# Kernel tuning notes

Measured on AMD Instinct MI355X. Metric: run time of the kernel, lower is better.

## Reference

```python
import jax, jax.numpy as jnp
import numpy as np

NIBBLE_SHIFTS = jnp.arange(8, dtype=jnp.int32) * 4


def _unpack_int4(packed):
    # packed: [..., P] int32 -> [..., P*8] int32 values in [0, 15]
    vals = (packed[..., None] >> NIBBLE_SHIFTS) & 0xF
    return vals.reshape(*packed.shape[:-1], packed.shape[-1] * 8)


def setup_inputs() -> dict:
    key = jax.random.key(0)
    k1, k2, k3, k4, k5, k6 = jax.random.split(key, 6)
    M, K, N, G = 4096, 4096, 11008, 128
    inp = jax.random.normal(k1, (M, K), dtype=jnp.float32)
    qweight = jax.random.randint(k2, (K, N // 8), 0, 2147483647, dtype=jnp.int32)
    woq_scales = jax.random.uniform(k3, (K // G, N), dtype=jnp.float32)
    woq_qzeros = jax.random.randint(k4, (K // G, N // 8), 0, 2147483647, dtype=jnp.int32)
    woq_bias = jax.random.normal(k5, (N,), dtype=jnp.float32)
    mul = jax.random.normal(k6, (M, N), dtype=jnp.float32)
    return {"inp": inp, "qweight": qweight, "woq_scales": woq_scales,
            "woq_qzeros": woq_qzeros, "woq_bias": woq_bias, "mul": mul,
            "group_size": G}


def reference(inp, qweight, woq_scales, woq_qzeros, woq_bias, mul, group_size):
    K = qweight.shape[0]
    # dequantize int4 weights: w = (q - z) * scale, per group of `group_size` K-rows
    w_int = _unpack_int4(qweight).astype(jnp.float32)            # [K, N]
    z_int = _unpack_int4(woq_qzeros).astype(jnp.float32)         # [K/G, N]
    zeros_full = jnp.repeat(z_int, group_size, axis=0)           # [K, N]
    scales_full = jnp.repeat(woq_scales, group_size, axis=0)     # [K, N]
    w = (w_int - zeros_full) * scales_full                       # [K, N]
    woq_out = inp @ w + woq_bias                                 # [M, N]
    return jax.nn.silu(woq_out) * mul
```

## Files before the change

kernel.cpp:

```cpp
#include <hip/hip_runtime.h>
#include <hip/hip_bf16.h>

typedef __attribute__((ext_vector_type(8))) short short8;
typedef __attribute__((ext_vector_type(4))) short short4v;
typedef __attribute__((ext_vector_type(4))) float float4v;

__device__ __forceinline__ short f2bf(float f) {
  union { float f; unsigned u; } v; v.f = f;
  unsigned r = v.u + 0x7fffu + ((v.u >> 16) & 1u);
  return (short)(r >> 16);
}

typedef const __attribute__((address_space(1))) unsigned int* as1_u32p;
typedef __attribute__((address_space(3))) unsigned int* as3_u32p;

__device__ __forceinline__ void gl_lds16(const void* g, void* l) {
  __builtin_amdgcn_global_load_lds((as1_u32p)g, (as3_u32p)l, 16, 0, 0);
}

__global__ __launch_bounds__(256, 2)
void dequant_kernel(const int* __restrict__ qw,
                    const float* __restrict__ scales,
                    const int* __restrict__ qzeros,
                    short* __restrict__ Bt,
                    int K, int N, int G)
{
  __shared__ short Ls[128 * 64];
  const int N8  = N >> 3;
  const int k0  = blockIdx.x * 64;
  const int n80 = blockIdx.y * 16;
  const int g   = k0 / G;
  const int tid  = threadIdx.x;
  const int lane = tid & 63;
  const int w    = tid >> 6;

  const int4 q4 = *(const int4*)(qw + (size_t)(k0 + lane) * N8 + n80 + w * 4);
  const int4 z4 = *(const int4*)(qzeros + (size_t)g * N8 + n80 + w * 4);
  const int qa[4] = {q4.x, q4.y, q4.z, q4.w};
  const int za[4] = {z4.x, z4.y, z4.z, z4.w};

  #pragma unroll
  for (int it = 0; it < 4; ++it) {
    const int n8l = w * 4 + it;
    const float4v s0 = *(const float4v*)(scales + (size_t)g * N + (n80 + n8l) * 8);
    const float4v s1 = *(const float4v*)(scales + (size_t)g * N + (n80 + n8l) * 8 + 4);
    const float sc[8] = {s0[0], s0[1], s0[2], s0[3], s1[0], s1[1], s1[2], s1[3]};
    const int wq = qa[it], wz = za[it];
    #pragma unroll
    for (int j = 0; j < 8; ++j) {
      const float z = (float)((wz >> (4 * j)) & 0xF);
      const float q = (float)((wq >> (4 * j)) & 0xF);
      Ls[(n8l * 8 + j) * 64 + lane] = f2bf((q - z) * sc[j]);
    }
  }
  __syncthreads();

  #pragma unroll
  for (int it = 0; it < 4; ++it) {
    const int c   = tid + it * 256;
    const int row = c >> 3;
    const int off = (c & 7) * 8;
    const short8 v = *(const short8*)(&Ls[row * 64 + off]);
    *(short8*)(Bt + (size_t)(n80 * 8 + row) * K + k0 + off) = v;
  }
}

__global__ __launch_bounds__(256, 4)
void aconv_kernel(const float* __restrict__ in, short* __restrict__ out, long long n)
{
  const long long i = ((long long)blockIdx.x * blockDim.x + threadIdx.x) * 8;
  if (i >= n) return;
  const float4v a = *(const float4v*)(in + i);
  const float4v b = *(const float4v*)(in + i + 4);
  short8 h;
  h[0] = f2bf(a[0]); h[1] = f2bf(a[1]); h[2] = f2bf(a[2]); h[3] = f2bf(a[3]);
  h[4] = f2bf(b[0]); h[5] = f2bf(b[1]); h[6] = f2bf(b[2]); h[7] = f2bf(b[3]);
  *(short8*)(out + i) = h;
}

__global__ __launch_bounds__(512, 2)
void gemm256_silu_mul_kernel(const short* __restrict__ A,
                             const short* __restrict__ Bt,
                             const float* __restrict__ bias,
                             const float* __restrict__ mulp,
                             float*       __restrict__ out,
                             int M, int N, int K)
{
  __shared__ short L[2][2][16384];

  const int tid  = threadIdx.x;
  const int lane = tid & 63;
  const int wave = tid >> 6;
  const int wm   = wave >> 2;
  const int wn   = wave & 3;

  const int nwg = gridDim.x;
  const int q8 = nwg >> 3, r8 = nwg & 7;
  const int xcd = blockIdx.x & 7, sub = blockIdx.x >> 3;
  const int swz = (xcd < r8 ? xcd * (q8 + 1) : r8 * (q8 + 1) + (xcd - r8) * q8) + sub;
  const int nbx = N >> 8;
  const int bx = swz % nbx, by = swz / nbx;
  const int m0 = by << 8, n0 = bx << 8;

  const short* Ab = A  + (size_t)m0 * K;
  const short* Bb = Bt + (size_t)n0 * K;

  const int srow = lane >> 2;
  const int scol = (((lane & 3) ^ ((lane & 32) >> 4))) * 8;
  const int fm = lane & 15;
  const int ko = ((lane >> 4) * 8) ^ ((fm & 8) ? 16 : 0);

  float4v acc[8][4];
  #pragma unroll
  for (int i = 0; i < 8; ++i)
    #pragma unroll
    for (int j = 0; j < 4; ++j)
      acc[i][j] = (float4v){0.f, 0.f, 0.f, 0.f};

  const int NT = K >> 6;

  auto stage = [&](int buf, int ab, const short* __restrict__ base, int kk) {
    #pragma unroll
    for (int i = 0; i < 4; ++i) {
      const int ms = wave * 2 + (i >> 1);
      const int ks = i & 1;
      const int st = ms * 2 + ks;
      gl_lds16(base + (size_t)(ms * 16 + srow) * K + kk + ks * 32 + scol,
               &L[buf][ab][st * 512]);
    }
  };

  stage(0, 0, Ab, 0);
  stage(0, 1, Bb, 0);

  for (int t = 0; t < NT; ++t) {
    const int cur = t & 1;
    const int kk1 = (t + 1) << 6;
    const bool pf = (t + 1) < NT;

    asm volatile("s_waitcnt vmcnt(0)" ::: "memory");
    __builtin_amdgcn_s_barrier();

    #pragma unroll
    for (int qm = 0; qm < 2; ++qm) {
      short8 af[4][2];
      #pragma unroll
      for (int i = 0; i < 4; ++i)
        #pragma unroll
        for (int ks = 0; ks < 2; ++ks)
          af[i][ks] = *(const short8*)(
              &L[cur][0][((wm * 8 + qm * 4 + i) * 2 + ks) * 512 + fm * 32 + ko]);

      #pragma unroll
      for (int qn = 0; qn < 2; ++qn) {
        short8 bf[2][2];
        #pragma unroll
        for (int j = 0; j < 2; ++j)
          #pragma unroll
          for (int ks = 0; ks < 2; ++ks)
            bf[j][ks] = *(const short8*)(
                &L[cur][1][((wn * 4 + qn * 2 + j) * 2 + ks) * 512 + fm * 32 + ko]);

        if (qm == 0 && pf) {
          if (qn == 0) stage(cur ^ 1, 0, Ab, kk1);
          else         stage(cur ^ 1, 1, Bb, kk1);
        }

        __builtin_amdgcn_s_barrier();
        asm volatile("s_waitcnt lgkmcnt(0)" ::: "memory");
        __builtin_amdgcn_sched_barrier(0);
        __builtin_amdgcn_s_setprio(1);
        #pragma unroll
        for (int i = 0; i < 4; ++i)
          #pragma unroll
          for (int j = 0; j < 2; ++j)
            #pragma unroll
            for (int ks = 0; ks < 2; ++ks)
              acc[qm * 4 + i][qn * 2 + j] = __builtin_amdgcn_mfma_f32_16x16x32_bf16(
                  af[i][ks], bf[j][ks], acc[qm * 4 + i][qn * 2 + j], 0, 0, 0);
        __builtin_amdgcn_s_setprio(0);
        __builtin_amdgcn_s_barrier();
      }
    }
  }

  const int cn  = lane & 15;
  const int cr4 = (lane >> 4) * 4;
  #pragma unroll
  for (int mt = 0; mt < 8; ++mt) {
    #pragma unroll
    for (int nt = 0; nt < 4; ++nt) {
      const int n  = n0 + wn * 64 + nt * 16 + cn;
      const float bn = bias[n];
      #pragma unroll
      for (int i = 0; i < 4; ++i) {
        const int m = m0 + wm * 128 + mt * 16 + cr4 + i;
        float x = acc[mt][nt][i] + bn;
        float s = x / (1.0f + __expf(-x));
        out[(size_t)m * N + n] = s * mulp[(size_t)m * N + n];
      }
    }
  }
}

__global__ __launch_bounds__(256, 2)
void gemm_silu_mul_kernel(const short* __restrict__ A,
                          const short* __restrict__ Bt,
                          const float* __restrict__ bias,
                          const float* __restrict__ mulp,
                          float*       __restrict__ out,
                          int M, int N, int K)
{
  __shared__ short As[128 * 64];
  __shared__ short Bs[128 * 64];

  const int tid  = threadIdx.x;
  const int lane = tid & 63;
  const int wave = tid >> 6;
  const int wr = (wave >> 1) * 64;
  const int wc = (wave & 1) * 64;
  const int m0 = blockIdx.y * 128;
  const int n0 = blockIdx.x * 128;

  float4v acc[4][4];
  #pragma unroll
  for (int i = 0; i < 4; ++i)
    #pragma unroll
    for (int j = 0; j < 4; ++j)
      acc[i][j] = (float4v){0.f, 0.f, 0.f, 0.f};

  const int fm = lane & 15;
  const int fk = (lane >> 4) * 8;
  const int srow = lane >> 3;
  const int scol = (lane & 7) * 8;

  for (int k0 = 0; k0 < K; k0 += 64) {
    #pragma unroll
    for (int c = 0; c < 4; ++c) {
      const int chunk = wave * 4 + c;
      const int row   = chunk * 8 + srow;
      gl_lds16(A  + (size_t)(m0 + row) * K + k0 + scol, &As[chunk * 512]);
      gl_lds16(Bt + (size_t)(n0 + row) * K + k0 + scol, &Bs[chunk * 512]);
    }
    __syncthreads();

    #pragma unroll
    for (int ks = 0; ks < 64; ks += 32) {
      short8 a[4], b[4];
      #pragma unroll
      for (int mt = 0; mt < 4; ++mt)
        a[mt] = *(const short8*)(&As[(wr + mt * 16 + fm) * 64 + ks + fk]);
      #pragma unroll
      for (int nt = 0; nt < 4; ++nt)
        b[nt] = *(const short8*)(&Bs[(wc + nt * 16 + fm) * 64 + ks + fk]);
      #pragma unroll
      for (int mt = 0; mt < 4; ++mt)
        #pragma unroll
        for (int nt = 0; nt < 4; ++nt)
          acc[mt][nt] = __builtin_amdgcn_mfma_f32_16x16x32_bf16(a[mt], b[nt], acc[mt][nt], 0, 0, 0);
    }
    __syncthreads();
  }

  const int cn = lane & 15;
  const int cr = (lane >> 4) * 4;
  #pragma unroll
  for (int mt = 0; mt < 4; ++mt) {
    #pragma unroll
    for (int nt = 0; nt < 4; ++nt) {
      const int n  = n0 + wc + nt * 16 + cn;
      const float bn = bias[n];
      #pragma unroll
      for (int i = 0; i < 4; ++i) {
        const int m = m0 + wr + mt * 16 + cr + i;
        float x = acc[mt][nt][i] + bn;
        float s = x / (1.0f + __expf(-x));
        out[(size_t)m * N + n] = s * mulp[(size_t)m * N + n];
      }
    }
  }
}

#define BM 128
#define BN 128
#define BK 64
#define LDA 72
#define LDB 72

__global__ __launch_bounds__(256, 2)
void woq_silu_mul_kernel(const float* __restrict__ inp, const int* __restrict__ qw,
                         const float* __restrict__ scales, const int* __restrict__ qzeros,
                         const float* __restrict__ bias, const float* __restrict__ mulp,
                         float* __restrict__ out, int M, int N, int K, int G)
{
  __shared__ short As[BM * LDA];
  __shared__ short Bs[BN * LDB];
  const int tid  = threadIdx.x;
  const int lane = tid & 63;
  const int wave = tid >> 6;
  const int wr = (wave >> 1) * 64;
  const int wc = (wave & 1) * 64;
  const int m0 = blockIdx.y * BM;
  const int n0 = blockIdx.x * BN;
  const int N8 = N >> 3;
  float4v acc[4][4];
  #pragma unroll
  for (int i = 0; i < 4; ++i)
    #pragma unroll
    for (int j = 0; j < 4; ++j)
      acc[i][j] = (float4v){0.f, 0.f, 0.f, 0.f};
  const int n8l  = tid >> 4;
  const int kloc = (tid & 15) * 4;
  const int fm = lane & 15;
  const int fk = (lane >> 4) * 8;
  for (int k0 = 0; k0 < K; k0 += BK) {
    #pragma unroll
    for (int i = 0; i < 8; ++i) {
      int f = tid + i * 256;
      int row = f >> 4;
      int col = (f & 15) * 4;
      float4v a4 = *(const float4v*)(inp + (size_t)(m0 + row) * K + k0 + col);
      short4v h;
      h[0] = f2bf(a4[0]); h[1] = f2bf(a4[1]); h[2] = f2bf(a4[2]); h[3] = f2bf(a4[3]);
      *(short4v*)(&As[row * LDA + col]) = h;
    }
    {
      const int g = k0 / G;
      const int n8g = (n0 >> 3) + n8l;
      const int zw = qzeros[(size_t)g * N8 + n8g];
      const float4v s0 = *(const float4v*)(scales + (size_t)g * N + n0 + n8l * 8);
      const float4v s1 = *(const float4v*)(scales + (size_t)g * N + n0 + n8l * 8 + 4);
      float sc[8] = {s0[0], s0[1], s0[2], s0[3], s1[0], s1[1], s1[2], s1[3]};
      int w[4];
      #pragma unroll
      for (int kk = 0; kk < 4; ++kk)
        w[kk] = qw[(size_t)(k0 + kloc + kk) * N8 + n8g];
      #pragma unroll
      for (int j = 0; j < 8; ++j) {
        const float zj = (float)((zw >> (4 * j)) & 0xF);
        const float sj = sc[j];
        short4v h;
        #pragma unroll
        for (int kk = 0; kk < 4; ++kk) {
          int q = (w[kk] >> (4 * j)) & 0xF;
          h[kk] = f2bf(((float)q - zj) * sj);
        }
        *(short4v*)(&Bs[(n8l * 8 + j) * LDB + kloc]) = h;
      }
    }
    __syncthreads();
    #pragma unroll
    for (int ks = 0; ks < BK; ks += 32) {
      short8 a[4], b[4];
      #pragma unroll
      for (int mt = 0; mt < 4; ++mt)
        a[mt] = *(const short8*)(&As[(wr + mt * 16 + fm) * LDA + ks + fk]);
      #pragma unroll
      for (int nt = 0; nt < 4; ++nt)
        b[nt] = *(const short8*)(&Bs[(wc + nt * 16 + fm) * LDB + ks + fk]);
      #pragma unroll
      for (int mt = 0; mt < 4; ++mt)
        #pragma unroll
        for (int nt = 0; nt < 4; ++nt)
          acc[mt][nt] = __builtin_amdgcn_mfma_f32_16x16x32_bf16(a[mt], b[nt], acc[mt][nt], 0, 0, 0);
    }
    __syncthreads();
  }
  const int cn = lane & 15;
  const int cr = (lane >> 4) * 4;
  #pragma unroll
  for (int mt = 0; mt < 4; ++mt) {
    #pragma unroll
    for (int nt = 0; nt < 4; ++nt) {
      const int n = n0 + wc + nt * 16 + cn;
      const float bn = bias[n];
      #pragma unroll
      for (int i = 0; i < 4; ++i) {
        const int m = m0 + wr + mt * 16 + cr + i;
        float x = acc[mt][nt][i] + bn;
        float s = x / (1.0f + __expf(-x));
        out[(size_t)m * N + n] = s * mulp[(size_t)m * N + n];
      }
    }
  }
}

extern "C" void kernel_launch(void* const* d_in, const int* in_sizes, int n_in,
                              void* d_out, int out_size, void* d_ws, size_t ws_size,
                              hipStream_t stream) {
  const float* inp    = (const float*)d_in[0];
  const int*   qw     = (const int*)d_in[1];
  const float* scales = (const float*)d_in[2];
  const int*   qzeros = (const int*)d_in[3];
  const float* bias   = (const float*)d_in[4];
  const float* mulp   = (const float*)d_in[5];
  float*       out    = (float*)d_out;

  const int N = in_sizes[4];
  const int K = (int)(((long long)in_sizes[1] * 8) / N);
  const int M = (int)((long long)in_sizes[0] / K);
  const int G = K / (in_sizes[2] / N);

  const size_t btBytes = (size_t)N * K * sizeof(short);
  const size_t aBytes  = (size_t)M * K * sizeof(short);

  if (ws_size >= btBytes + aBytes) {
    short* Bt  = (short*)d_ws;
    short* Abf = (short*)((char*)d_ws + btBytes);

    dim3 dq_grid(K / 64, (N / 8) / 16);
    dequant_kernel<<<dq_grid, dim3(256), 0, stream>>>(qw, scales, qzeros, Bt, K, N, G);

    const long long nA = (long long)M * K;
    aconv_kernel<<<dim3((unsigned)((nA / 8 + 255) / 256)), dim3(256), 0, stream>>>(inp, Abf, nA);

    if ((M & 255) == 0 && (N & 255) == 0 && (K & 63) == 0) {
      dim3 grid((unsigned)((N >> 8) * (M >> 8)));
      gemm256_silu_mul_kernel<<<grid, dim3(512), 0, stream>>>(Abf, Bt, bias, mulp, out, M, N, K);
    } else {
      dim3 grid(N / 128, M / 128);
      gemm_silu_mul_kernel<<<grid, dim3(256), 0, stream>>>(Abf, Bt, bias, mulp, out, M, N, K);
    }
  } else {
    dim3 grid(N / BN, M / BM);
    woq_silu_mul_kernel<<<grid, dim3(256), 0, stream>>>(inp, qw, scales, qzeros,
                                                        bias, mulp, out, M, N, K, G);
  }
}
```

Measured before the change: 728.0 us.

## Reorder GEMM main loop into four quadrant phases with finer-grained prefetch waits

Restructures the bf16 MFMA main loop so each K-step runs four quadrant phases (top-left, top-right, bottom-left, bottom-right). Fragments are reused across phases, and the next tile is prefetched in per-group chunks, with partial vmcnt waits replacing the full drain at the top of every iteration. The aim is to overlap global-to-LDS loads with MFMA work and stop stalling on all outstanding loads each K-step. The cost is more barriers and tighter reasoning about which LDS groups are complete, which raises the risk of races if the wait counts do not match the load order.

```diff
diff --git a/kernel.cpp b/kernel.cpp
--- a/kernel.cpp
+++ b/kernel.cpp
@@ -110,6 +110,11 @@
   const int fm = lane & 15;
   const int ko = ((lane >> 4) * 8) ^ ((fm & 8) ? 16 : 0);
 
+  const int BG0 = wave * 2;
+  const int BG1 = wave * 2 + 1;
+  const int AEg = (wave & 3) + (wave >> 2) * 8;
+  const int ALg = AEg + 4;
+
   float4v acc[8][4];
   #pragma unroll
   for (int i = 0; i < 8; ++i)
@@ -119,69 +124,116 @@
 
   const int NT = K >> 6;
 
-  auto stage = [&](int buf, int ab, const short* __restrict__ base, int kk) {
-    #pragma unroll
-    for (int i = 0; i < 4; ++i) {
-      const int ms = wave * 2 + (i >> 1);
-      const int ks = i & 1;
-      const int st = ms * 2 + ks;
-      gl_lds16(base + (size_t)(ms * 16 + srow) * K + kk + ks * 32 + scol,
-               &L[buf][ab][st * 512]);
-    }
+  auto stage2 = [&](int buf, int ab, int g, const short* __restrict__ base, int kk) {
+    #pragma unroll
+    for (int ks = 0; ks < 2; ++ks)
+      gl_lds16(base + (size_t)(g * 16 + srow) * K + kk + ks * 32 + scol,
+               &L[buf][ab][(g * 2 + ks) * 512]);
   };
 
-  stage(0, 0, Ab, 0);
-  stage(0, 1, Bb, 0);
+  stage2(0, 1, BG0, Bb, 0);
+  stage2(0, 1, BG1, Bb, 0);
+  stage2(0, 0, AEg, Ab, 0);
+  stage2(0, 0, ALg, Ab, 0);
+  asm volatile("s_waitcnt vmcnt(2)" ::: "memory");
+  __builtin_amdgcn_s_barrier();
 
   for (int t = 0; t < NT; ++t) {
     const int cur = t & 1;
+    const int nxt = cur ^ 1;
     const int kk1 = (t + 1) << 6;
     const bool pf = (t + 1) < NT;
 
-    asm volatile("s_waitcnt vmcnt(0)" ::: "memory");
-    __builtin_amdgcn_s_barrier();
-
-    #pragma unroll
-    for (int qm = 0; qm < 2; ++qm) {
-      short8 af[4][2];
-      #pragma unroll
-      for (int i = 0; i < 4; ++i)
+    short8 af[4][2], bf[4][2];
+
+    #pragma unroll
+    for (int i = 0; i < 4; ++i)
+      #pragma unroll
+      for (int ks = 0; ks < 2; ++ks)
+        af[i][ks] = *(const short8*)(
+            &L[cur][0][((wm * 8 + i) * 2 + ks) * 512 + fm * 32 + ko]);
+    #pragma unroll
+    for (int j = 0; j < 2; ++j)
+      #pragma unroll
+      for (int ks = 0; ks < 2; ++ks)
+        bf[j][ks] = *(const short8*)(
+            &L[cur][1][((wn * 4 + j) * 2 + ks) * 512 + fm * 32 + ko]);
+    if (pf) stage2(nxt, 1, BG0, Bb, kk1);
+    __builtin_amdgcn_s_barrier();
+    asm volatile("s_waitcnt lgkmcnt(0)" ::: "memory");
+    __builtin_amdgcn_sched_barrier(0);
+    __builtin_amdgcn_s_setprio(1);
+    #pragma unroll
+    for (int i = 0; i < 4; ++i)
+      #pragma unroll
+      for (int j = 0; j < 2; ++j)
         #pragma unroll
         for (int ks = 0; ks < 2; ++ks)
-          af[i][ks] = *(const short8*)(
-              &L[cur][0][((wm * 8 + qm * 4 + i) * 2 + ks) * 512 + fm * 32 + ko]);
-
-      #pragma unroll
-      for (int qn = 0; qn < 2; ++qn) {
-        short8 bf[2][2];
-        #pragma unroll
-        for (int j = 0; j < 2; ++j)
-          #pragma unroll
-          for (int ks = 0; ks < 2; ++ks)
-            bf[j][ks] = *(const short8*)(
-                &L[cur][1][((wn * 4 + qn * 2 + j) * 2 + ks) * 512 + fm * 32 + ko]);
-
-        if (qm == 0 && pf) {
-          if (qn == 0) stage(cur ^ 1, 0, Ab, kk1);
-          else         stage(cur ^ 1, 1, Bb, kk1);
-        }
-
-        __builtin_amdgcn_s_barrier();
-        asm volatile("s_waitcnt lgkmcnt(0)" ::: "memory");
-        __builtin_amdgcn_sched_barrier(0);
-        __builtin_amdgcn_s_setprio(1);
-        #pragma unroll
-        for (int i = 0; i < 4; ++i)
-          #pragma unroll
-          for (int j = 0; j < 2; ++j)
-            #pragma unroll
-            for (int ks = 0; ks < 2; ++ks)
-              acc[qm * 4 + i][qn * 2 + j] = __builtin_amdgcn_mfma_f32_16x16x32_bf16(
-                  af[i][ks], bf[j][ks], acc[qm * 4 + i][qn * 2 + j], 0, 0, 0);
-        __builtin_amdgcn_s_setprio(0);
-        __builtin_amdgcn_s_barrier();
-      }
-    }
+          acc[i][j] = __builtin_amdgcn_mfma_f32_16x16x32_bf16(
+              af[i][ks], bf[j][ks], acc[i][j], 0, 0, 0);
+    __builtin_amdgcn_s_setprio(0);
+    __builtin_amdgcn_s_barrier();
+
+    #pragma unroll
+    for (int j = 2; j < 4; ++j)
+      #pragma unroll
+      for (int ks = 0; ks < 2; ++ks)
+        bf[j][ks] = *(const short8*)(
+            &L[cur][1][((wn * 4 + j) * 2 + ks) * 512 + fm * 32 + ko]);
+    if (pf) stage2(nxt, 1, BG1, Bb, kk1);
+    __builtin_amdgcn_s_barrier();
+    asm volatile("s_waitcnt lgkmcnt(0)" ::: "memory");
+    __builtin_amdgcn_sched_barrier(0);
+    __builtin_amdgcn_s_setprio(1);
+    #pragma unroll
+    for (int i = 0; i < 4; ++i)
+      #pragma unroll
+      for (int j = 2; j < 4; ++j)
+        #pragma unroll
+        for (int ks = 0; ks < 2; ++ks)
+          acc[i][j] = __builtin_amdgcn_mfma_f32_16x16x32_bf16(
+              af[i][ks], bf[j][ks], acc[i][j], 0, 0, 0);
+    __builtin_amdgcn_s_setprio(0);
+    if (pf) { asm volatile("s_waitcnt vmcnt(4)" ::: "memory"); }
+    else    { asm volatile("s_waitcnt vmcnt(0)" ::: "memory"); }
+    __builtin_amdgcn_s_barrier();
+
+    #pragma unroll
+    for (int i = 0; i < 4; ++i)
+      #pragma unroll
+      for (int ks = 0; ks < 2; ++ks)
+        af[i][ks] = *(const short8*)(
+            &L[cur][0][((wm * 8 + 4 + i) * 2 + ks) * 512 + fm * 32 + ko]);
+    if (pf) stage2(nxt, 0, AEg, Ab, kk1);
+    __builtin_amdgcn_s_barrier();
+    asm volatile("s_waitcnt lgkmcnt(0)" ::: "memory");
+    __builtin_amdgcn_sched_barrier(0);
+    __builtin_amdgcn_s_setprio(1);
+    #pragma unroll
+    for (int i = 0; i < 4; ++i)
+      #pragma unroll
+      for (int j = 0; j < 2; ++j)
+        #pragma unroll
+        for (int ks = 0; ks < 2; ++ks)
+          acc[4 + i][j] = __builtin_amdgcn_mfma_f32_16x16x32_bf16(
+              af[i][ks], bf[j][ks], acc[4 + i][j], 0, 0, 0);
+    __builtin_amdgcn_s_setprio(0);
+    __builtin_amdgcn_s_barrier();
+
+    if (pf) stage2(nxt, 0, ALg, Ab, kk1);
+    __builtin_amdgcn_s_barrier();
+    __builtin_amdgcn_s_setprio(1);
+    #pragma unroll
+    for (int i = 0; i < 4; ++i)
+      #pragma unroll
+      for (int j = 2; j < 4; ++j)
+        #pragma unroll
+        for (int ks = 0; ks < 2; ++ks)
+          acc[4 + i][j] = __builtin_amdgcn_mfma_f32_16x16x32_bf16(
+              af[i][ks], bf[j][ks], acc[4 + i][j], 0, 0, 0);
+    __builtin_amdgcn_s_setprio(0);
+    if (pf) { asm volatile("s_waitcnt vmcnt(2)" ::: "memory"); }
+    __builtin_amdgcn_s_barrier();
   }
 
   const int cn  = lane & 15;
```

Result: faster. 699.9 us (-3.9%).

## Fuse int4 dequantization into the 256x256 GEMM mainloop, dropping separate dequant pass

Applied to the files above, without the earlier changes.

Removes the standalone dequant kernel and the bf16 weight buffer. The GEMM now loads packed int4 weights, zeros and scales per tile, dequantizes them in registers and writes the bf16 B tile into LDS, overlapping this with the MFMA work. The tile raster order switches to M-major and the finer barrier/priority scheduling is replaced by a single syncthreads per k-step. In exchange, every M-tile re-reads and re-dequantizes the weights (M/256 times), uses scalar uncoalesced int32 loads, and adds VALU work inside the mainloop.

```diff
diff --git a/kernel.cpp b/kernel.cpp
--- a/kernel.cpp
+++ b/kernel.cpp
@@ -16,53 +16,6 @@
 
 __device__ __forceinline__ void gl_lds16(const void* g, void* l) {
   __builtin_amdgcn_global_load_lds((as1_u32p)g, (as3_u32p)l, 16, 0, 0);
-}
-
-__global__ __launch_bounds__(256, 2)
-void dequant_kernel(const int* __restrict__ qw,
-                    const float* __restrict__ scales,
-                    const int* __restrict__ qzeros,
-                    short* __restrict__ Bt,
-                    int K, int N, int G)
-{
-  __shared__ short Ls[128 * 64];
-  const int N8  = N >> 3;
-  const int k0  = blockIdx.x * 64;
-  const int n80 = blockIdx.y * 16;
-  const int g   = k0 / G;
-  const int tid  = threadIdx.x;
-  const int lane = tid & 63;
-  const int w    = tid >> 6;
-
-  const int4 q4 = *(const int4*)(qw + (size_t)(k0 + lane) * N8 + n80 + w * 4);
-  const int4 z4 = *(const int4*)(qzeros + (size_t)g * N8 + n80 + w * 4);
-  const int qa[4] = {q4.x, q4.y, q4.z, q4.w};
-  const int za[4] = {z4.x, z4.y, z4.z, z4.w};
-
-  #pragma unroll
-  for (int it = 0; it < 4; ++it) {
-    const int n8l = w * 4 + it;
-    const float4v s0 = *(const float4v*)(scales + (size_t)g * N + (n80 + n8l) * 8);
-    const float4v s1 = *(const float4v*)(scales + (size_t)g * N + (n80 + n8l) * 8 + 4);
-    const float sc[8] = {s0[0], s0[1], s0[2], s0[3], s1[0], s1[1], s1[2], s1[3]};
-    const int wq = qa[it], wz = za[it];
-    #pragma unroll
-    for (int j = 0; j < 8; ++j) {
-      const float z = (float)((wz >> (4 * j)) & 0xF);
-      const float q = (float)((wq >> (4 * j)) & 0xF);
-      Ls[(n8l * 8 + j) * 64 + lane] = f2bf((q - z) * sc[j]);
-    }
-  }
-  __syncthreads();
-
-  #pragma unroll
-  for (int it = 0; it < 4; ++it) {
-    const int c   = tid + it * 256;
-    const int row = c >> 3;
-    const int off = (c & 7) * 8;
-    const short8 v = *(const short8*)(&Ls[row * 64 + off]);
-    *(short8*)(Bt + (size_t)(n80 * 8 + row) * K + k0 + off) = v;
-  }
 }
 
 __global__ __launch_bounds__(256, 4)
@@ -79,12 +32,14 @@
 }
 
 __global__ __launch_bounds__(512, 2)
-void gemm256_silu_mul_kernel(const short* __restrict__ A,
-                             const short* __restrict__ Bt,
-                             const float* __restrict__ bias,
-                             const float* __restrict__ mulp,
-                             float*       __restrict__ out,
-                             int M, int N, int K)
+void gemm256_woq_kernel(const short* __restrict__ A,
+                        const int* __restrict__ qw,
+                        const float* __restrict__ scales,
+                        const int* __restrict__ qzeros,
+                        const float* __restrict__ bias,
+                        const float* __restrict__ mulp,
+                        float* __restrict__ out,
+                        int M, int N, int K, int G)
 {
   __shared__ short L[2][2][16384];
 
@@ -98,18 +53,26 @@
   const int q8 = nwg >> 3, r8 = nwg & 7;
   const int xcd = blockIdx.x & 7, sub = blockIdx.x >> 3;
   const int swz = (xcd < r8 ? xcd * (q8 + 1) : r8 * (q8 + 1) + (xcd - r8) * q8) + sub;
-  const int nbx = N >> 8;
-  const int bx = swz % nbx, by = swz / nbx;
+  const int nby = M >> 8;
+  const int by = swz % nby, bx = swz / nby;
   const int m0 = by << 8, n0 = bx << 8;
 
-  const short* Ab = A  + (size_t)m0 * K;
-  const short* Bb = Bt + (size_t)n0 * K;
+  const int N8  = N >> 3;
+  const int n80 = n0 >> 3;
+  const short* Ab = A + (size_t)m0 * K;
 
   const int srow = lane >> 2;
   const int scol = (((lane & 3) ^ ((lane & 32) >> 4))) * 8;
   const int fm = lane & 15;
   const int ko = ((lane >> 4) * 8) ^ ((fm & 8) ? 16 : 0);
 
+  const int rr = lane >> 2;
+  const int cc = lane & 3;
+  const int hi = rr >> 3;
+  const int kc = cc ^ (hi ? 2 : 0);
+  const int jj = rr & 7;
+  const int j4 = jj * 4;
+
   float4v acc[8][4];
   #pragma unroll
   for (int i = 0; i < 8; ++i)
@@ -119,69 +82,103 @@
 
   const int NT = K >> 6;
 
-  auto stage = [&](int buf, int ab, const short* __restrict__ base, int kk) {
-    #pragma unroll
-    for (int i = 0; i < 4; ++i) {
-      const int ms = wave * 2 + (i >> 1);
-      const int ks = i & 1;
-      const int st = ms * 2 + ks;
-      gl_lds16(base + (size_t)(ms * 16 + srow) * K + kk + ks * 32 + scol,
-               &L[buf][ab][st * 512]);
+  auto stageA = [&](int buf, int kk) {
+    #pragma unroll
+    for (int gi = 0; gi < 2; ++gi) {
+      const int g = wave * 2 + gi;
+      #pragma unroll
+      for (int ks = 0; ks < 2; ++ks)
+        gl_lds16(Ab + (size_t)(g * 16 + srow) * K + kk + ks * 32 + scol,
+                 &L[buf][0][(g * 2 + ks) * 512]);
     }
   };
 
-  stage(0, 0, Ab, 0);
-  stage(0, 1, Bb, 0);
+  auto loadQW = [&](int b, int kk, int gg, int (&qd)[2][8], int& zq, float& sc) {
+    const int n8c = n80 + (wave * 2 + b) * 2 + hi;
+    #pragma unroll
+    for (int ks = 0; ks < 2; ++ks)
+      #pragma unroll
+      for (int u = 0; u < 8; ++u)
+        qd[ks][u] = qw[(size_t)(kk + ks * 32 + kc * 8 + u) * N8 + n8c];
+    zq = qzeros[(size_t)gg * N8 + n8c];
+    sc = scales[(size_t)gg * N + n8c * 8 + jj];
+  };
+
+  auto deqWrite = [&](int buf, int b, const int (&qd)[2][8], int zq, float sc) {
+    const float zf = (float)((zq >> j4) & 0xF);
+    #pragma unroll
+    for (int ks = 0; ks < 2; ++ks) {
+      short8 h;
+      #pragma unroll
+      for (int u = 0; u < 8; ++u) {
+        const float qf = (float)((qd[ks][u] >> j4) & 0xF);
+        h[u] = f2bf((qf - zf) * sc);
+      }
+      *(short8*)(&L[buf][1][(((wave * 2 + b) * 2 + ks) * 512) + lane * 8]) = h;
+    }
+  };
+
+  {
+    int qd0[2][8], qd1[2][8]; int zq0, zq1; float sc0, sc1;
+    stageA(0, 0);
+    loadQW(0, 0, 0, qd0, zq0, sc0);
+    loadQW(1, 0, 0, qd1, zq1, sc1);
+    deqWrite(0, 0, qd0, zq0, sc0);
+    deqWrite(0, 1, qd1, zq1, sc1);
+  }
+  __syncthreads();
 
   for (int t = 0; t < NT; ++t) {
-    const int cur = t & 1;
+    const int cur = t & 1, nxt = cur ^ 1;
+    const bool pf = (t + 1) < NT;
     const int kk1 = (t + 1) << 6;
-    const bool pf = (t + 1) < NT;
-
-    asm volatile("s_waitcnt vmcnt(0)" ::: "memory");
-    __builtin_amdgcn_s_barrier();
-
-    #pragma unroll
-    for (int qm = 0; qm < 2; ++qm) {
-      short8 af[4][2];
-      #pragma unroll
-      for (int i = 0; i < 4; ++i)
+    const int g1  = kk1 / G;
+
+    int qd0[2][8], qd1[2][8]; int zq0 = 0, zq1 = 0; float sc0 = 0.f, sc1 = 0.f;
+    if (pf) { stageA(nxt, kk1); loadQW(0, kk1, g1, qd0, zq0, sc0); }
+
+    short8 af[4][2], bf[4][2];
+    #pragma unroll
+    for (int j = 0; j < 4; ++j)
+      #pragma unroll
+      for (int ks = 0; ks < 2; ++ks)
+        bf[j][ks] = *(const short8*)(
+            &L[cur][1][((wn * 4 + j) * 2 + ks) * 512 + fm * 32 + ko]);
+    #pragma unroll
+    for (int i = 0; i < 4; ++i)
+      #pragma unroll
+      for (int ks = 0; ks < 2; ++ks)
+        af[i][ks] = *(const short8*)(
+            &L[cur][0][((wm * 8 + i) * 2 + ks) * 512 + fm * 32 + ko]);
+    #pragma unroll
+    for (int i = 0; i < 4; ++i)
+      #pragma unroll
+      for (int j = 0; j < 4; ++j)
         #pragma unroll
         for (int ks = 0; ks < 2; ++ks)
-          af[i][ks] = *(const short8*)(
-              &L[cur][0][((wm * 8 + qm * 4 + i) * 2 + ks) * 512 + fm * 32 + ko]);
-
-      #pragma unroll
-      for (int qn = 0; qn < 2; ++qn) {
-        short8 bf[2][2];
+          acc[i][j] = __builtin_amdgcn_mfma_f32_16x16x32_bf16(
+              af[i][ks], bf[j][ks], acc[i][j], 0, 0, 0);
+
+    if (pf) { loadQW(1, kk1, g1, qd1, zq1, sc1); deqWrite(nxt, 0, qd0, zq0, sc0); }
+
+    #pragma unroll
+    for (int i = 0; i < 4; ++i)
+      #pragma unroll
+      for (int ks = 0; ks < 2; ++ks)
+        af[i][ks] = *(const short8*)(
+            &L[cur][0][((wm * 8 + 4 + i) * 2 + ks) * 512 + fm * 32 + ko]);
+    #pragma unroll
+    for (int i = 0; i < 4; ++i)
+      #pragma unroll
+      for (int j = 0; j < 4; ++j)
         #pragma unroll
-        for (int j = 0; j < 2; ++j)
-          #pragma unroll
-          for (int ks = 0; ks < 2; ++ks)
-            bf[j][ks] = *(const short8*)(
-                &L[cur][1][((wn * 4 + qn * 2 + j) * 2 + ks) * 512 + fm * 32 + ko]);
-
-        if (qm == 0 && pf) {
-          if (qn == 0) stage(cur ^ 1, 0, Ab, kk1);
-          else         stage(cur ^ 1, 1, Bb, kk1);
-        }
-
-        __builtin_amdgcn_s_barrier();
-        asm volatile("s_waitcnt lgkmcnt(0)" ::: "memory");
-        __builtin_amdgcn_sched_barrier(0);
-        __builtin_amdgcn_s_setprio(1);
-        #pragma unroll
-        for (int i = 0; i < 4; ++i)
-          #pragma unroll
-          for (int j = 0; j < 2; ++j)
-            #pragma unroll
-            for (int ks = 0; ks < 2; ++ks)
-              acc[qm * 4 + i][qn * 2 + j] = __builtin_amdgcn_mfma_f32_16x16x32_bf16(
-                  af[i][ks], bf[j][ks], acc[qm * 4 + i][qn * 2 + j], 0, 0, 0);
-        __builtin_amdgcn_s_setprio(0);
-        __builtin_amdgcn_s_barrier();
-      }
-    }
+        for (int ks = 0; ks < 2; ++ks)
+          acc[4 + i][j] = __builtin_amdgcn_mfma_f32_16x16x32_bf16(
+              af[i][ks], bf[j][ks], acc[4 + i][j], 0, 0, 0);
+
+    if (pf) { deqWrite(nxt, 1, qd1, zq1, sc1); }
+
+    __syncthreads();
   }
 
   const int cn  = lane & 15;
@@ -200,6 +197,53 @@
         out[(size_t)m * N + n] = s * mulp[(size_t)m * N + n];
       }
     }
+  }
+}
+
+__global__ __launch_bounds__(256, 2)
+void dequant_kernel_v0(const int* __restrict__ qw,
+                       const float* __restrict__ scales,
+                       const int* __restrict__ qzeros,
+                       short* __restrict__ Bt,
+                       int K, int N, int G)
+{
+  __shared__ short Ls[128 * 64];
+  const int N8  = N >> 3;
+  const int k0  = blockIdx.x * 64;
+  const int n80 = blockIdx.y * 16;
+  const int g   = k0 / G;
+  const int tid  = threadIdx.x;
+  const int lane = tid & 63;
+  const int w    = tid >> 6;
+
+  const int4 q4 = *(const int4*)(qw + (size_t)(k0 + lane) * N8 + n80 + w * 4);
+  const int4 z4 = *(const int4*)(qzeros + (size_t)g * N8 + n80 + w * 4);
+  const int qa[4] = {q4.x, q4.y, q4.z, q4.w};
+  const int za[4] = {z4.x, z4.y, z4.z, z4.w};
+
+  #pragma unroll
+  for (int it = 0; it < 4; ++it) {
+    const int n8l = w * 4 + it;
+    const float4v s0 = *(const float4v*)(scales + (size_t)g * N + (n80 + n8l) * 8);
+    const float4v s1 = *(const float4v*)(scales + (size_t)g * N + (n80 + n8l) * 8 + 4);
+    const float sc[8] = {s0[0], s0[1], s0[2], s0[3], s1[0], s1[1], s1[2], s1[3]};
+    const int wq = qa[it], wz = za[it];
+    #pragma unroll
+    for (int j = 0; j < 8; ++j) {
+      const float z = (float)((wz >> (4 * j)) & 0xF);
+      const float q = (float)((wq >> (4 * j)) & 0xF);
+      Ls[(n8l * 8 + j) * 64 + lane] = f2bf((q - z) * sc[j]);
+    }
+  }
+  __syncthreads();
+
+  #pragma unroll
+  for (int it = 0; it < 4; ++it) {
+    const int c   = tid + it * 256;
+    const int row = c >> 3;
+    const int off = (c & 7) * 8;
+    const short8 v = *(const short8*)(&Ls[row * 64 + off]);
+    *(short8*)(Bt + (size_t)(n80 * 8 + row) * K + k0 + off) = v;
   }
 }
 
@@ -403,24 +447,26 @@
 
   const size_t btBytes = (size_t)N * K * sizeof(short);
   const size_t aBytes  = (size_t)M * K * sizeof(short);
-
-  if (ws_size >= btBytes + aBytes) {
+  const long long nA = (long long)M * K;
+
+  const bool fusedOk = (M & 255) == 0 && (N & 255) == 0 && (K & 63) == 0 &&
+                       G >= 64 && (G & 63) == 0 && (nA & 7) == 0 && K >= 64;
+
+  if (fusedOk && ws_size >= aBytes) {
+    short* Abf = (short*)d_ws;
+    aconv_kernel<<<dim3((unsigned)((nA / 8 + 255) / 256)), dim3(256), 0, stream>>>(inp, Abf, nA);
+    dim3 grid((unsigned)((N >> 8) * (M >> 8)));
+    gemm256_woq_kernel<<<grid, dim3(512), 0, stream>>>(
+        Abf, qw, scales, qzeros, bias, mulp, out, M, N, K, G);
+  } else if (ws_size >= btBytes + aBytes && (M & 127) == 0 && (N & 127) == 0 &&
+             (K & 63) == 0 && (nA & 7) == 0) {
     short* Bt  = (short*)d_ws;
     short* Abf = (short*)((char*)d_ws + btBytes);
-
     dim3 dq_grid(K / 64, (N / 8) / 16);
-    dequant_kernel<<<dq_grid, dim3(256), 0, stream>>>(qw, scales, qzeros, Bt, K, N, G);
-
-    const long long nA = (long long)M * K;
+    dequant_kernel_v0<<<dq_grid, dim3(256), 0, stream>>>(qw, scales, qzeros, Bt, K, N, G);
     aconv_kernel<<<dim3((unsigned)((nA / 8 + 255) / 256)), dim3(256), 0, stream>>>(inp, Abf, nA);
-
-    if ((M & 255) == 0 && (N & 255) == 0 && (K & 63) == 0) {
-      dim3 grid((unsigned)((N >> 8) * (M >> 8)));
-      gemm256_silu_mul_kernel<<<grid, dim3(512), 0, stream>>>(Abf, Bt, bias, mulp, out, M, N, K);
-    } else {
-      dim3 grid(N / 128, M / 128);
-      gemm_silu_mul_kernel<<<grid, dim3(256), 0, stream>>>(Abf, Bt, bias, mulp, out, M, N, K);
-    }
+    dim3 grid(N / 128, M / 128);
+    gemm_silu_mul_kernel<<<grid, dim3(256), 0, stream>>>(Abf, Bt, bias, mulp, out, M, N, K);
   } else {
     dim3 grid(N / BN, M / BM);
     woq_silu_mul_kernel<<<grid, dim3(256), 0, stream>>>(inp, qw, scales, qzeros,
```

Measured after the change: 1.966 ms. 170% more time.
